# Optimization experiments

Hardware: AMD Instinct MI355X
Metric: run time of the kernel (lower is better)

Reference implementation:

```python
import jax, jax.numpy as jnp
import numpy as np

D = 1024
H = 8
B = 16384
TYPES = 3


def _mha(q_in, k_in, v_in, Wq, bq, Wk, bk, Wv, bv, Wo, bo, num_heads):
    """Manual multi-head attention matching the torch modules (eval mode, no dropout).
    q_in/k_in/v_in: [B, S, D]. Weights used as x @ W + b (equivalent param'n of nn.Linear).
    """
    b, s, d = q_in.shape
    hd = d // num_heads
    q = (q_in @ Wq + bq).reshape(b, s, num_heads, hd)
    k = (k_in @ Wk + bk).reshape(b, s, num_heads, hd)
    v = (v_in @ Wv + bv).reshape(b, s, num_heads, hd)
    scores = jnp.einsum('bqhd,bkhd->bhqk', q, k) / jnp.sqrt(jnp.asarray(hd, q.dtype))
    w = jax.nn.softmax(scores, axis=-1)
    out = jnp.einsum('bhqk,bkhd->bqhd', w, v).reshape(b, s, d)
    return out @ Wo + bo


def setup_inputs() -> dict:
    key = jax.random.key(0)
    ks = jax.random.split(key, 16)
    s = 0.02
    inp = {
        'drug_a': jax.random.normal(ks[0], (B, D), jnp.float32),
        'drug_b': jax.random.normal(ks[1], (B, D), jnp.float32),
        # stacked params for the 4 attention blocks: 0=sa_a, 1=sa_b, 2=ca_ab, 3=ca_ba
        'Wq': jax.random.normal(ks[2], (4, D, D), jnp.float32) * s,
        'bq': jnp.zeros((4, D), jnp.float32),
        'Wk': jax.random.normal(ks[3], (4, D, D), jnp.float32) * s,
        'bk': jnp.zeros((4, D), jnp.float32),
        'Wv': jax.random.normal(ks[4], (4, D, D), jnp.float32) * s,
        'bv': jnp.zeros((4, D), jnp.float32),
        'Wo': jax.random.normal(ks[5], (4, D, D), jnp.float32) * s,
        'bo': jnp.zeros((4, D), jnp.float32),
        'Wc': jax.random.normal(ks[6], (2 * D, TYPES), jnp.float32) * s,
        'bc': jnp.zeros((TYPES,), jnp.float32),
        'Wg': jax.random.normal(ks[7], (2 * D, D), jnp.float32) * s,
        'bg': jnp.zeros((D,), jnp.float32),
    }
    return inp


def reference(drug_a, drug_b, Wq, bq, Wk, bk, Wv, bv, Wo, bo, Wc, bc, Wg, bg):
    a_seq = drug_a[:, None, :]  # [B, 1, D]
    b_seq = drug_b[:, None, :]

    a_att = _mha(a_seq, a_seq, a_seq, Wq[0], bq[0], Wk[0], bk[0], Wv[0], bv[0], Wo[0], bo[0], H)[:, 0]
    b_att = _mha(b_seq, b_seq, b_seq, Wq[1], bq[1], Wk[1], bk[1], Wv[1], bv[1], Wo[1], bo[1], H)[:, 0]
    a_cross = _mha(a_seq, b_seq, b_seq, Wq[2], bq[2], Wk[2], bk[2], Wv[2], bv[2], Wo[2], bo[2], H)[:, 0]
    b_cross = _mha(b_seq, a_seq, a_seq, Wq[3], bq[3], Wk[3], bk[3], Wv[3], bv[3], Wo[3], bo[3], H)[:, 0]

    combined = jnp.concatenate([a_cross, b_cross], axis=1)  # [B, 2D]
    interaction_logits = combined @ Wc + bc                  # [B, TYPES]
    gate = jax.nn.sigmoid(combined @ Wg + bg)                # [B, D]
    fused = (a_att + b_att) * gate
    return fused, interaction_logits
```

## Files before the change

### kernel.cpp

```cpp
#include <hip/hip_runtime.h>


typedef unsigned short ushort_t;
typedef __attribute__((ext_vector_type(4))) float f32x4;
typedef __attribute__((ext_vector_type(8))) __bf16 bf16x8;

__device__ __forceinline__ unsigned short f2bf(float f) {
    unsigned int u = __float_as_uint(f);
    u = (u + 0x7fffu + ((u >> 16) & 1u)) >> 16;
    return (unsigned short)u;
}
__device__ __forceinline__ float bf2f(unsigned int u) {
    return __uint_as_float(u << 16);
}

__device__ __forceinline__ void gload16(const void* g, void* l) {
    __builtin_amdgcn_global_load_lds(
        (const __attribute__((address_space(1))) void*)g,
        (__attribute__((address_space(3))) void*)l, 16, 0, 0);
}

__device__ __forceinline__ f32x4 mfma16(bf16x8 a, bf16x8 b, f32x4 c) {
    return __builtin_amdgcn_mfma_f32_16x16x32_bf16(a, b, c, 0, 0, 0);
}


__global__ __launch_bounds__(256) void convA_kernel(
    const float* __restrict__ a, const float* __restrict__ b,
    ushort_t* __restrict__ Abf) {
    int idx = blockIdx.x * 256 + threadIdx.x;
    size_t e0 = (size_t)idx * 8;
    int i = (int)(e0 >> 11);
    int k = (int)(e0 & 2047);
    const float* src = (k < 1024) ? (a + (size_t)i * 1024 + k)
                                  : (b + (size_t)i * 1024 + (k - 1024));
    float4 f0 = ((const float4*)src)[0];
    float4 f1 = ((const float4*)src)[1];
    uint4 o;
    o.x = (unsigned)f2bf(f0.x) | ((unsigned)f2bf(f0.y) << 16);
    o.y = (unsigned)f2bf(f0.z) | ((unsigned)f2bf(f0.w) << 16);
    o.z = (unsigned)f2bf(f1.x) | ((unsigned)f2bf(f1.y) << 16);
    o.w = (unsigned)f2bf(f1.z) | ((unsigned)f2bf(f1.w) << 16);
    *(uint4*)(Abf + e0) = o;
}

__global__ __launch_bounds__(256) void convC_kernel(
    const float* __restrict__ src, ushort_t* __restrict__ dst) {
    size_t e0 = ((size_t)blockIdx.x * 256 + threadIdx.x) * 8;
    float4 f0 = ((const float4*)(src + e0))[0];
    float4 f1 = ((const float4*)(src + e0))[1];
    uint4 o;
    o.x = (unsigned)f2bf(f0.x) | ((unsigned)f2bf(f0.y) << 16);
    o.y = (unsigned)f2bf(f0.z) | ((unsigned)f2bf(f0.w) << 16);
    o.z = (unsigned)f2bf(f1.x) | ((unsigned)f2bf(f1.y) << 16);
    o.w = (unsigned)f2bf(f1.z) | ((unsigned)f2bf(f1.w) << 16);
    *(uint4*)(dst + e0) = o;
}

__global__ __launch_bounds__(256) void convT_kernel(
    const float* __restrict__ src, ushort_t* __restrict__ dst,
    int R, int C, long zs, long zd) {
    __shared__ float tile[32][33];
    int tx = threadIdx.x & 31, ty = threadIdx.x >> 5;
    const float* s = src + (size_t)blockIdx.z * zs;
    ushort_t* d = dst + (size_t)blockIdx.z * zd;
    int r0 = blockIdx.y * 32, c0 = blockIdx.x * 32;
#pragma unroll
    for (int p = 0; p < 4; ++p)
        tile[p * 8 + ty][tx] = s[(size_t)(r0 + p * 8 + ty) * C + c0 + tx];
    __syncthreads();
#pragma unroll
    for (int p = 0; p < 4; ++p)
        d[(size_t)(c0 + p * 8 + ty) * R + r0 + tx] = f2bf(tile[tx][p * 8 + ty]);
}


__global__ __launch_bounds__(256) void biasT2_kernel(
    const float* __restrict__ bv, const float* __restrict__ Wo,
    const float* __restrict__ bo, float* __restrict__ t4) {
    int bx = blockIdx.x;
    int g = bx >> 5, jt = (bx >> 3) & 3, kc = bx & 7;
    int j = jt * 256 + threadIdx.x;
    const float* W = Wo + (size_t)g * 1048576;
    const float* v = bv + g * 1024;
    float acc = (kc == 0) ? bo[g * 1024 + j] : 0.f;
    int k0 = kc * 128;
    for (int k = k0; k < k0 + 128; ++k)
        acc += v[k] * W[(size_t)k * 1024 + j];
    atomicAdd(&t4[g * 1024 + j], acc);
}

__global__ __launch_bounds__(256) void post_kernel(
    const float* __restrict__ t4, const float* __restrict__ Wg,
    const float* __restrict__ bg, const float* __restrict__ Wc,
    const float* __restrict__ bc, float* __restrict__ cG,
    float* __restrict__ cC) {
    if (blockIdx.x < 64) {
        int jt = blockIdx.x >> 4, kc = blockIdx.x & 15;
        int j = jt * 256 + threadIdx.x;
        float acc = (kc == 0) ? bg[j] : 0.f;
        int k0 = kc * 128;
        for (int k = k0; k < k0 + 128; ++k)
            acc += t4[2048 + k] * Wg[(size_t)k * 1024 + j];
        atomicAdd(&cG[j], acc);
    } else {
        __shared__ float red[192];
        int tid = threadIdx.x;
        if (tid < 192) {
            int t = tid % 3, c = tid / 3;
            float acc = 0.f;
            for (int kk = 0; kk < 32; ++kk) {
                int k = c * 32 + kk;
                acc += t4[2048 + k] * Wc[(size_t)k * 3 + t];
            }
            red[tid] = acc;
        }
        __syncthreads();
        if (tid < 3) {
            float s = bc[tid];
            for (int c = 0; c < 64; ++c) s += red[tid + 3 * c];
            cC[tid] = s;
        }
    }
}

__global__ __launch_bounds__(256) void lfold2_kernel(
    const ushort_t* __restrict__ Mbuf, const float* __restrict__ Wc,
    float* __restrict__ Lw) {
    int wid = blockIdx.x * 4 + (threadIdx.x >> 6);
    int l = threadIdx.x & 63;
    int h = wid >> 10, k = wid & 1023;
    const ushort_t* Mrow = Mbuf + (h == 0 ? 1048576 : 0) + (size_t)k * 1024;
    const float* Wcp = Wc + (h == 0 ? 3072 : 0);
    float a0 = 0.f, a1 = 0.f, a2 = 0.f;
#pragma unroll 4
    for (int i = 0; i < 16; ++i) {
        int m = i * 64 + l;
        float x = bf2f((unsigned)Mrow[m]);
        const float* wp = Wcp + (size_t)m * 3;
        a0 += x * wp[0];
        a1 += x * wp[1];
        a2 += x * wp[2];
    }
#pragma unroll
    for (int off = 32; off; off >>= 1) {
        a0 += __shfl_xor(a0, off);
        a1 += __shfl_xor(a1, off);
        a2 += __shfl_xor(a2, off);
    }
    if (l == 0) {
        float* o = Lw + (size_t)(h * 1024 + k) * 3;
        o[0] = a0; o[1] = a1; o[2] = a2;
    }
}

__device__ __forceinline__ void fold_body(
    ushort_t* sA, ushort_t* sB,
    const ushort_t* __restrict__ A, int lda,
    const ushort_t* __restrict__ BT, int ldbt,
    ushort_t* __restrict__ ob, int ldout, int rowMode, int colOff,
    int bx, int by) {
    int tid = threadIdx.x, w = tid >> 6, l = tid & 63;
    f32x4 acc[2][4];
#pragma unroll
    for (int i = 0; i < 2; ++i)
#pragma unroll
        for (int j = 0; j < 4; ++j) acc[i][j] = (f32x4){0.f, 0.f, 0.f, 0.f};
    int srow = l >> 3, skoff = (l & 7) * 8;
    const ushort_t* Abase = A + (size_t)(by * 64 + w * 32 + srow) * lda + skoff;
    const ushort_t* Bbase = BT + (size_t)(bx * 64 + w * 32 + srow) * ldbt + skoff;
    for (int k0 = 0; k0 < 1024; k0 += 64) {
        __syncthreads();
#pragma unroll
        for (int i = 0; i < 4; ++i) {
            gload16(Abase + (size_t)i * 8 * lda + k0, &sA[(w * 32 + i * 8) * 64]);
            gload16(Bbase + (size_t)i * 8 * ldbt + k0, &sB[(w * 32 + i * 8) * 64]);
        }
        __syncthreads();
#pragma unroll
        for (int kk = 0; kk < 2; ++kk) {
            int kb = kk * 32 + (l >> 4) * 8;
            bf16x8 aF[2], bF[4];
#pragma unroll
            for (int mi = 0; mi < 2; ++mi)
                aF[mi] = *(const bf16x8*)&sA[(w * 32 + mi * 16 + (l & 15)) * 64 + kb];
#pragma unroll
            for (int ni = 0; ni < 4; ++ni)
                bF[ni] = *(const bf16x8*)&sB[(ni * 16 + (l & 15)) * 64 + kb];
#pragma unroll
            for (int mi = 0; mi < 2; ++mi)
#pragma unroll
                for (int ni = 0; ni < 4; ++ni)
                    acc[mi][ni] = mfma16(aF[mi], bF[ni], acc[mi][ni]);
        }
    }
    int col16 = l & 15, rg = (l >> 4) * 4;
#pragma unroll
    for (int mi = 0; mi < 2; ++mi)
#pragma unroll
        for (int ni = 0; ni < 4; ++ni) {
            int n = bx * 64 + ni * 16 + col16;
#pragma unroll
            for (int r = 0; r < 4; ++r) {
                int m = by * 64 + w * 32 + mi * 16 + rg + r;
                int orow = (rowMode == 0)
                               ? m
                               : ((m >> 6) * 128 + (rowMode == 2 ? 64 : 0) + (m & 63));
                ob[(size_t)orow * ldout + colOff + n] = f2bf(acc[mi][ni][r]);
            }
        }
}

__global__ __launch_bounds__(128) void fold_l12(
    const ushort_t* __restrict__ Wvbf, const ushort_t* __restrict__ WoT,
    ushort_t* __restrict__ WT, ushort_t* __restrict__ Mbuf) {
    __shared__ alignas(16) ushort_t sA[64 * 64];
    __shared__ alignas(16) ushort_t sB[64 * 64];
    int z = blockIdx.z;
    const ushort_t *A, *BT;
    ushort_t* ob;
    int rowMode, colOff, ldout;
    if (z < 2) {
        A = WoT + (size_t)z * 1048576;
        BT = Wvbf + (size_t)z * 1048576;
        ob = WT; rowMode = 1; colOff = z * 1024; ldout = 2048;
    } else {
        A = Wvbf + (size_t)z * 1048576;
        BT = WoT + (size_t)z * 1048576;
        ob = Mbuf + (size_t)(z - 2) * 1048576; rowMode = 0; colOff = 0; ldout = 1024;
    }
    fold_body(sA, sB, A, 1024, BT, 1024, ob, ldout, rowMode, colOff,
              blockIdx.x, blockIdx.y);
}

__global__ __launch_bounds__(128) void fold_l34(
    const ushort_t* __restrict__ WgT, const ushort_t* __restrict__ Mbuf,
    ushort_t* __restrict__ WT) {
    __shared__ alignas(16) ushort_t sA[64 * 64];
    __shared__ alignas(16) ushort_t sB[64 * 64];
    int z = blockIdx.z;
    const ushort_t* A = WgT + (z == 0 ? 1024 : 0);
    const ushort_t* BT = Mbuf + (z == 0 ? 1048576 : 0);
    fold_body(sA, sB, A, 2048, BT, 1024, WT, 2048, 2, z * 1024,
              blockIdx.x, blockIdx.y);
}

__global__ __launch_bounds__(256) void main_mm(
    const ushort_t* __restrict__ A, const ushort_t* __restrict__ WT,
    const float* __restrict__ t4, const float* __restrict__ cG,
    float* __restrict__ out) {
    __shared__ alignas(16) ushort_t sA[128 * 64];
    __shared__ alignas(16) ushort_t sB[128 * 64];
    int tid = threadIdx.x, w = tid >> 6, l = tid & 63;
    int bid = blockIdx.x;
    int swz = ((bid & 7) << 8) | (bid >> 3);
    int mt = swz >> 4, nt = swz & 15;
    size_t m0 = (size_t)mt * 128;
    f32x4 accL[2][4], accG[2][4];
#pragma unroll
    for (int i = 0; i < 2; ++i)
#pragma unroll
        for (int j = 0; j < 4; ++j) {
            accL[i][j] = (f32x4){0.f, 0.f, 0.f, 0.f};
            accG[i][j] = (f32x4){0.f, 0.f, 0.f, 0.f};
        }
    int srow = l >> 3, skoff = (l & 7) * 8;
    const ushort_t* Abase = A + (m0 + w * 32 + srow) * 2048 + skoff;
    const ushort_t* Bbase = WT + ((size_t)nt * 128 + w * 32 + srow) * 2048 + skoff;
    for (int k0 = 0; k0 < 2048; k0 += 64) {
        __syncthreads();
#pragma unroll
        for (int i = 0; i < 4; ++i) {
            gload16(Abase + (size_t)i * 8 * 2048 + k0, &sA[(w * 32 + i * 8) * 64]);
            gload16(Bbase + (size_t)i * 8 * 2048 + k0, &sB[(w * 32 + i * 8) * 64]);
        }
        __syncthreads();
#pragma unroll
        for (int kk = 0; kk < 2; ++kk) {
            int kb = kk * 32 + (l >> 4) * 8;
            bf16x8 aF[2], bF[8];
#pragma unroll
            for (int mi = 0; mi < 2; ++mi)
                aF[mi] = *(const bf16x8*)&sA[(w * 32 + mi * 16 + (l & 15)) * 64 + kb];
#pragma unroll
            for (int ni = 0; ni < 8; ++ni)
                bF[ni] = *(const bf16x8*)&sB[(ni * 16 + (l & 15)) * 64 + kb];
#pragma unroll
            for (int mi = 0; mi < 2; ++mi)
#pragma unroll
                for (int ni = 0; ni < 4; ++ni) {
                    accL[mi][ni] = mfma16(aF[mi], bF[ni], accL[mi][ni]);
                    accG[mi][ni] = mfma16(aF[mi], bF[4 + ni], accG[mi][ni]);
                }
        }
    }
    int col16 = l & 15, rg = (l >> 4) * 4;
#pragma unroll
    for (int mi = 0; mi < 2; ++mi)
#pragma unroll
        for (int ni = 0; ni < 4; ++ni) {
            int j = nt * 64 + ni * 16 + col16;
            float cl = t4[j] + t4[1024 + j];
            float cg = cG[j];
            size_t row0 = m0 + w * 32 + mi * 16 + rg;
#pragma unroll
            for (int r = 0; r < 4; ++r) {
                float lin = accL[mi][ni][r] + cl;
                float gv = accG[mi][ni][r] + cg;
                float s = 1.0f / (1.0f + __expf(-gv));
                out[(row0 + r) * 1024 + j] = lin * s;
            }
        }
}

__global__ __launch_bounds__(256) void logits_kernel(
    const ushort_t* __restrict__ Abf, const float* __restrict__ Lw,
    const float* __restrict__ cC, float* __restrict__ out) {
    __shared__ float LwS[3][2048];
    int tid = threadIdx.x;
    for (int idx = tid; idx < 6144; idx += 256) {
        int k = idx / 3, t = idx - 3 * k;
        LwS[t][k] = Lw[idx];
    }
    __syncthreads();
    int w = tid >> 6, l = tid & 63;
    float c0 = cC[0], c1 = cC[1], c2 = cC[2];
    for (int r = 0; r < 4; ++r) {
        int row = blockIdx.x * 16 + w * 4 + r;
        const ushort_t* Ar = Abf + (size_t)row * 2048;
        float a0 = 0.f, a1 = 0.f, a2 = 0.f;
#pragma unroll
        for (int i = 0; i < 16; ++i) {
            int k = 2 * l + 128 * i;
            unsigned int x = *(const unsigned int*)(Ar + k);
            float x0 = bf2f(x & 0xffffu), x1 = bf2f(x >> 16);
            float2 w0 = *(const float2*)&LwS[0][k];
            float2 w1 = *(const float2*)&LwS[1][k];
            float2 w2 = *(const float2*)&LwS[2][k];
            a0 += x0 * w0.x + x1 * w0.y;
            a1 += x0 * w1.x + x1 * w1.y;
            a2 += x0 * w2.x + x1 * w2.y;
        }
#pragma unroll
        for (int off = 32; off; off >>= 1) {
            a0 += __shfl_xor(a0, off);
            a1 += __shfl_xor(a1, off);
            a2 += __shfl_xor(a2, off);
        }
        if (l == 0) {
            size_t ob = (size_t)16777216 + (size_t)row * 3;
            out[ob] = a0 + c0;
            out[ob + 1] = a1 + c1;
            out[ob + 2] = a2 + c2;
        }
    }
}

extern "C" void kernel_launch(void* const* d_in, const int* in_sizes, int n_in,
                              void* d_out, int out_size, void* d_ws, size_t ws_size,
                              hipStream_t stream) {
    const float* dA = (const float*)d_in[0];
    const float* dB = (const float*)d_in[1];
    const float* Wv = (const float*)d_in[6];
    const float* bv = (const float*)d_in[7];
    const float* Wo = (const float*)d_in[8];
    const float* bo = (const float*)d_in[9];
    const float* Wc = (const float*)d_in[10];
    const float* bc = (const float*)d_in[11];
    const float* Wg = (const float*)d_in[12];
    const float* bg = (const float*)d_in[13];
    float* out = (float*)d_out;

    char* ws = (char*)d_ws;
    ushort_t* Abf  = (ushort_t*)(ws);
    ushort_t* WT   = (ushort_t*)(ws + 67108864);
    ushort_t* Wvbf = (ushort_t*)(ws + 75497472);
    ushort_t* WoT  = (ushort_t*)(ws + 83886080);
    ushort_t* WgT  = (ushort_t*)(ws + 92274688);
    ushort_t* Mbuf = (ushort_t*)(ws + 96468992);
    float* t4   = (float*)(ws + 100663296);
    float* cG   = (float*)(ws + 100683776);
    float* cC   = (float*)(ws + 100687872);
    float* Lw   = (float*)(ws + 100688128);

    convA_kernel<<<16384, 256, 0, stream>>>(dA, dB, Abf);
    convC_kernel<<<2048, 256, 0, stream>>>(Wv, Wvbf);
    convT_kernel<<<dim3(32, 32, 4), 256, 0, stream>>>(Wo, WoT, 1024, 1024, 1048576, 1048576);
    convT_kernel<<<dim3(32, 64, 1), 256, 0, stream>>>(Wg, WgT, 2048, 1024, 0, 0);
    hipMemsetAsync(ws + 100663296, 0, 24832, stream);
    biasT2_kernel<<<128, 256, 0, stream>>>(bv, Wo, bo, t4);
    fold_l12<<<dim3(16, 16, 4), 128, 0, stream>>>(Wvbf, WoT, WT, Mbuf);
    fold_l34<<<dim3(16, 16, 2), 128, 0, stream>>>(WgT, Mbuf, WT);
    post_kernel<<<65, 256, 0, stream>>>(t4, Wg, bg, Wc, bc, cG, cC);
    lfold2_kernel<<<512, 256, 0, stream>>>(Mbuf, Wc, Lw);
    main_mm<<<2048, 256, 0, stream>>>(Abf, WT, t4, cG, out);
    logits_kernel<<<1024, 256, 0, stream>>>(Abf, Lw, cC, out);
}
```

Before: 492.2 us.

## Rewrite main GEMM with 256x256 tiles, double-buffered LDS, and swizzled layout

The main fused linear+gate GEMM now uses 256x256 output tiles per 512-thread block instead of 128x128 per 256-thread block. Global-to-LDS loads are double-buffered and interleaved with MFMA phases, and the LDS columns are XOR-swizzled to avoid bank conflicts. The folded weight row interleave changes from 64-row to 32-row groups so that each wave's N slice holds both its linear and gate columns. This targets load latency and global traffic through larger reuse, at the cost of much more LDS (128KB per block) and more accumulator registers, with fewer blocks in flight.

Result: faster. 435.3 us (-11.5%).

```diff
diff --git a/kernel.cpp b/kernel.cpp
--- a/kernel.cpp
+++ b/kernel.cpp
@@ -205,7 +205,7 @@
                 int m = by * 64 + w * 32 + mi * 16 + rg + r;
                 int orow = (rowMode == 0)
                                ? m
-                               : ((m >> 6) * 128 + (rowMode == 2 ? 64 : 0) + (m & 63));
+                               : ((m >> 5) * 64 + (rowMode == 2 ? 32 : 0) + (m & 31));
                 ob[(size_t)orow * ldout + colOff + n] = f2bf(acc[mi][ni][r]);
             }
         }
@@ -245,72 +245,122 @@
               blockIdx.x, blockIdx.y);
 }
 
-__global__ __launch_bounds__(256) void main_mm(
+__global__ __launch_bounds__(512, 2) void main_mm(
     const ushort_t* __restrict__ A, const ushort_t* __restrict__ WT,
     const float* __restrict__ t4, const float* __restrict__ cG,
     float* __restrict__ out) {
-    __shared__ alignas(16) ushort_t sA[128 * 64];
-    __shared__ alignas(16) ushort_t sB[128 * 64];
-    int tid = threadIdx.x, w = tid >> 6, l = tid & 63;
-    int bid = blockIdx.x;
-    int swz = ((bid & 7) << 8) | (bid >> 3);
-    int mt = swz >> 4, nt = swz & 15;
-    size_t m0 = (size_t)mt * 128;
-    f32x4 accL[2][4], accG[2][4];
-#pragma unroll
-    for (int i = 0; i < 2; ++i)
-#pragma unroll
-        for (int j = 0; j < 4; ++j) {
-            accL[i][j] = (f32x4){0.f, 0.f, 0.f, 0.f};
-            accG[i][j] = (f32x4){0.f, 0.f, 0.f, 0.f};
-        }
-    int srow = l >> 3, skoff = (l & 7) * 8;
-    const ushort_t* Abase = A + (m0 + w * 32 + srow) * 2048 + skoff;
-    const ushort_t* Bbase = WT + ((size_t)nt * 128 + w * 32 + srow) * 2048 + skoff;
-    for (int k0 = 0; k0 < 2048; k0 += 64) {
-        __syncthreads();
-#pragma unroll
-        for (int i = 0; i < 4; ++i) {
-            gload16(Abase + (size_t)i * 8 * 2048 + k0, &sA[(w * 32 + i * 8) * 64]);
-            gload16(Bbase + (size_t)i * 8 * 2048 + k0, &sB[(w * 32 + i * 8) * 64]);
-        }
-        __syncthreads();
-#pragma unroll
-        for (int kk = 0; kk < 2; ++kk) {
-            int kb = kk * 32 + (l >> 4) * 8;
-            bf16x8 aF[2], bF[8];
-#pragma unroll
-            for (int mi = 0; mi < 2; ++mi)
-                aF[mi] = *(const bf16x8*)&sA[(w * 32 + mi * 16 + (l & 15)) * 64 + kb];
-#pragma unroll
-            for (int ni = 0; ni < 8; ++ni)
-                bF[ni] = *(const bf16x8*)&sB[(ni * 16 + (l & 15)) * 64 + kb];
-#pragma unroll
-            for (int mi = 0; mi < 2; ++mi)
+    __shared__ alignas(16) ushort_t sA[2][256 * 64];
+    __shared__ alignas(16) ushort_t sB[2][256 * 64];
+    const int tid = threadIdx.x;
+    const int w = tid >> 6, l = tid & 63;
+    const int wr = w >> 2, wc = w & 3;
+    const int bid = blockIdx.x;
+    const int idx = (bid & 7) * 64 + (bid >> 3);
+    const int mt = idx >> 3, ntb = idx & 7;
+    const size_t m0 = (size_t)mt * 256;
+    const size_t n0 = (size_t)ntb * 256;
+
+    const int csrc = (((l & 7) ^ (l >> 3)) * 8);
+    const ushort_t* gA0 = A  + (m0 + w * 16 + (l >> 3)) * 2048 + csrc;
+    const ushort_t* gB0 = WT + (n0 + w * 16 + (l >> 3)) * 2048 + csrc;
+
+#define STAGE_A(b, h, ko)                                                      \
+    do {                                                                       \
+        gload16(gA0 + (size_t)(h) * 262144 + (ko),                             \
+                &sA[b][((h) * 128 + w * 16) * 64]);                            \
+        gload16(gA0 + (size_t)(h) * 262144 + 16384 + (ko),                     \
+                &sA[b][((h) * 128 + w * 16 + 8) * 64]);                        \
+    } while (0)
+#define STAGE_B(b, h, ko)                                                      \
+    do {                                                                       \
+        gload16(gB0 + (size_t)(h) * 262144 + (ko),                             \
+                &sB[b][((h) * 128 + w * 16) * 64]);                            \
+        gload16(gB0 + (size_t)(h) * 262144 + 16384 + (ko),                     \
+                &sB[b][((h) * 128 + w * 16 + 8) * 64]);                        \
+    } while (0)
+
+    const int rbA = wr * 128 + (l & 15);
+    const int rbB = wc * 64 + (l & 15);
+    const int cxor = (l & 7) << 3;
+    const int c0 = ((l >> 4) * 8) ^ cxor;
+    const int c1 = (32 + (l >> 4) * 8) ^ cxor;
+
+    f32x4 acc[8][4];
+#pragma unroll
+    for (int i = 0; i < 8; ++i)
+#pragma unroll
+        for (int j = 0; j < 4; ++j) acc[i][j] = (f32x4){0.f, 0.f, 0.f, 0.f};
+
+    STAGE_A(0, 0, 0); STAGE_A(0, 1, 0); STAGE_B(0, 0, 0); STAGE_B(0, 1, 0);
+    asm volatile("s_waitcnt vmcnt(0)" ::: "memory");
+    __builtin_amdgcn_s_barrier();
+
+#pragma unroll 2
+    for (int t = 0; t < 32; ++t) {
+        const int cur = t & 1, nxt = cur ^ 1;
+        const int ko = (t + 1) * 64;
+        bf16x8 bF[4][2];
+#pragma unroll
+        for (int p = 0; p < 4; ++p) {
+            bf16x8 aF[2][2];
+            if (p == 0) {
 #pragma unroll
                 for (int ni = 0; ni < 4; ++ni) {
-                    accL[mi][ni] = mfma16(aF[mi], bF[ni], accL[mi][ni]);
-                    accG[mi][ni] = mfma16(aF[mi], bF[4 + ni], accG[mi][ni]);
+                    bF[ni][0] = *(const bf16x8*)&sB[cur][(rbB + ni * 16) * 64 + c0];
+                    bF[ni][1] = *(const bf16x8*)&sB[cur][(rbB + ni * 16) * 64 + c1];
                 }
-        }
-    }
-    int col16 = l & 15, rg = (l >> 4) * 4;
-#pragma unroll
-    for (int mi = 0; mi < 2; ++mi)
-#pragma unroll
-        for (int ni = 0; ni < 4; ++ni) {
-            int j = nt * 64 + ni * 16 + col16;
-            float cl = t4[j] + t4[1024 + j];
-            float cg = cG[j];
-            size_t row0 = m0 + w * 32 + mi * 16 + rg;
+            }
+#pragma unroll
+            for (int mil = 0; mil < 2; ++mil) {
+                aF[mil][0] = *(const bf16x8*)&sA[cur][(rbA + (2 * p + mil) * 16) * 64 + c0];
+                aF[mil][1] = *(const bf16x8*)&sA[cur][(rbA + (2 * p + mil) * 16) * 64 + c1];
+            }
+            if (t < 31) {
+                if (p == 0)      STAGE_A(nxt, 0, ko);
+                else if (p == 1) STAGE_A(nxt, 1, ko);
+                else if (p == 2) STAGE_B(nxt, 0, ko);
+                else             STAGE_B(nxt, 1, ko);
+            }
+            __builtin_amdgcn_s_barrier();
+            asm volatile("s_waitcnt lgkmcnt(0)" ::: "memory");
+            __builtin_amdgcn_sched_barrier(0);
+            __builtin_amdgcn_s_setprio(1);
+#pragma unroll
+            for (int mil = 0; mil < 2; ++mil)
+#pragma unroll
+                for (int ni = 0; ni < 4; ++ni) {
+                    acc[2 * p + mil][ni] = mfma16(aF[mil][0], bF[ni][0], acc[2 * p + mil][ni]);
+                    acc[2 * p + mil][ni] = mfma16(aF[mil][1], bF[ni][1], acc[2 * p + mil][ni]);
+                }
+            __builtin_amdgcn_s_setprio(0);
+            __builtin_amdgcn_sched_barrier(0);
+            if (p < 3) __builtin_amdgcn_s_barrier();
+        }
+        asm volatile("s_waitcnt vmcnt(0)" ::: "memory");
+        __builtin_amdgcn_s_barrier();
+    }
+
+    const int col16 = l & 15, rg = (l >> 4) * 4;
+    const int g2 = ntb * 4 + wc;
+#pragma unroll
+    for (int ni = 0; ni < 2; ++ni) {
+        const int j = g2 * 32 + ni * 16 + col16;
+        const float cl = t4[j] + t4[1024 + j];
+        const float cg = cG[j];
+#pragma unroll
+        for (int mi = 0; mi < 8; ++mi) {
+            const size_t row0 = m0 + wr * 128 + mi * 16 + rg;
 #pragma unroll
             for (int r = 0; r < 4; ++r) {
-                float lin = accL[mi][ni][r] + cl;
-                float gv = accG[mi][ni][r] + cg;
+                float lin = acc[mi][ni][r] + cl;
+                float gv = acc[mi][ni + 2][r] + cg;
                 float s = 1.0f / (1.0f + __expf(-gv));
                 out[(row0 + r) * 1024 + j] = lin * s;
             }
         }
+    }
+#undef STAGE_A
+#undef STAGE_B
 }
 
 __global__ __launch_bounds__(256) void logits_kernel(
@@ -393,6 +443,6 @@
     fold_l34<<<dim3(16, 16, 2), 128, 0, stream>>>(WgT, Mbuf, WT);
     post_kernel<<<65, 256, 0, stream>>>(t4, Wg, bg, Wc, bc, cG, cC);
     lfold2_kernel<<<512, 256, 0, stream>>>(Mbuf, Wc, Lw);
-    main_mm<<<2048, 256, 0, stream>>>(Abf, WT, t4, cG, out);
+    main_mm<<<512, 512, 0, stream>>>(Abf, WT, t4, cG, out);
     logits_kernel<<<1024, 256, 0, stream>>>(Abf, Lw, cC, out);
 }
```
